# Performance work log

Measured on AMD Instinct MI355X. Metric: run time of the kernel, lower is better.

Reference implementation:

```python
import jax, jax.numpy as jnp
import numpy as np

N_NODES = 10000
N_EDGES = 320000
HIDDEN = 256
HEADS = 8
HEAD_DIM = HIDDEN // HEADS  # 32
NEG_SLOPE = 0.2


def setup_inputs() -> dict:
    key = jax.random.key(0)
    ks = jax.random.split(key, 12)
    x = jax.random.normal(ks[0], (N_NODES, HIDDEN), dtype=jnp.float32)
    edges_idx = jax.random.randint(ks[1], (2, N_EDGES), 0, N_NODES, dtype=jnp.int64)
    s = 1.0 / np.sqrt(HIDDEN)
    # layer 1 params
    W1 = jax.random.normal(ks[2], (HIDDEN, HEADS * HEAD_DIM), dtype=jnp.float32) * s
    a_src1 = jax.random.normal(ks[3], (HEADS, HEAD_DIM), dtype=jnp.float32) * s
    a_dst1 = jax.random.normal(ks[4], (HEADS, HEAD_DIM), dtype=jnp.float32) * s
    b1 = jnp.zeros((HEADS * HEAD_DIM,), dtype=jnp.float32)
    # layer 2 params
    W2 = jax.random.normal(ks[5], (HIDDEN, HEADS * HEAD_DIM), dtype=jnp.float32) * s
    a_src2 = jax.random.normal(ks[6], (HEADS, HEAD_DIM), dtype=jnp.float32) * s
    a_dst2 = jax.random.normal(ks[7], (HEADS, HEAD_DIM), dtype=jnp.float32) * s
    b2 = jnp.zeros((HEADS * HEAD_DIM,), dtype=jnp.float32)
    return {"x": x, "edges_idx": edges_idx,
            "W1": W1, "a_src1": a_src1, "a_dst1": a_dst1, "b1": b1,
            "W2": W2, "a_src2": a_src2, "a_dst2": a_dst2, "b2": b2}


def gat_conv(x, src, dst, W, a_src, a_dst, b):
    """PyG GATConv (concat=True, negative_slope=0.2), dropout in eval mode."""
    N = x.shape[0]
    h = (x @ W).reshape(N, HEADS, HEAD_DIM)          # [N,H,C]
    alpha_s = jnp.einsum('nhc,hc->nh', h, a_src)     # [N,H]
    alpha_d = jnp.einsum('nhc,hc->nh', h, a_dst)     # [N,H]
    e = alpha_s[src] + alpha_d[dst]                  # [E,H]
    e = jnp.where(e > 0, e, NEG_SLOPE * e)           # leaky_relu
    # scatter-softmax over incoming edges of each dst node
    m = jax.ops.segment_max(e, dst, num_segments=N)  # [N,H]
    ex = jnp.exp(e - m[dst])                         # [E,H]
    denom = jax.ops.segment_sum(ex, dst, num_segments=N)  # [N,H]
    alpha = ex / (denom[dst] + 1e-16)                # [E,H]
    msg = h[src] * alpha[:, :, None]                 # [E,H,C]
    out = jax.ops.segment_sum(msg, dst, num_segments=N)   # [N,H,C]
    return out.reshape(N, HEADS * HEAD_DIM) + b


def reference(x, edges_idx, W1, a_src1, a_dst1, b1, W2, a_src2, a_dst2, b2):
    src = edges_idx[0]
    dst = edges_idx[1]
    h = gat_conv(x, src, dst, W1, a_src1, a_dst1, b1)
    h = jax.nn.elu(h)
    out = gat_conv(h, src, dst, W2, a_src2, a_dst2, b2)
    return out
```

## Files before the change

kernel.cpp:

```cpp
#include <hip/hip_runtime.h>
#include <hip/hip_bf16.h>
#include <hip/hip_fp16.h>

#define N_NODES 10000
#define N_EDGES 320000
#define HIDDEN 256
#define HEADS 8
#define HEAD_DIM 32
#define NEG_SLOPE 0.2f
#define CAP 80

typedef __attribute__((ext_vector_type(8))) short short8;
typedef __attribute__((ext_vector_type(8))) _Float16 half8;
typedef __attribute__((ext_vector_type(4))) float f32x4;

__device__ __forceinline__ void bf16_split(float v, unsigned short& hi, unsigned short& lo) {
    __hip_bfloat16 hb = __float2bfloat16(v);
    float hf = __bfloat162float(hb);
    __hip_bfloat16 lb = __float2bfloat16(v - hf);
    hi = *reinterpret_cast<unsigned short*>(&hb);
    lo = *reinterpret_cast<unsigned short*>(&lb);
}

__global__ __launch_bounds__(256) void prep_kernel(
    const float* __restrict__ W1, const float* __restrict__ W2,
    const int* __restrict__ src, const int* __restrict__ dst,
    unsigned short* __restrict__ w1h, unsigned short* __restrict__ w1l,
    unsigned short* __restrict__ w2h, unsigned short* __restrict__ w2l,
    int* __restrict__ counts, int* __restrict__ csr_src) {
    int b = blockIdx.x;
    int tid = threadIdx.x;
    if (b < 512) {
        int i = b * 256 + tid;
        int which = i >> 16;
        int rem = i & 0xFFFF;
        int k = rem >> 8, n = rem & 255;
        const float* W = which ? W2 : W1;
        unsigned short* wh = which ? w2h : w1h;
        unsigned short* wl = which ? w2l : w1l;
        unsigned short h, l;
        bf16_split(W[k * 256 + n], h, l);
        wh[n * 256 + k] = h;
        wl[n * 256 + k] = l;
    } else {
        int e = (b - 512) * 256 + tid;
        int d = dst[e];
        int rank = atomicAdd(&counts[d], 1);
        csr_src[d * CAP + rank] = src[e];
    }
}

template <int AFP32>
__global__ __launch_bounds__(512) void gemm_mfma_kernel(
    const float* __restrict__ Axf,
    const unsigned short* __restrict__ Ah, const unsigned short* __restrict__ Al,
    const unsigned short* __restrict__ BhT, const unsigned short* __restrict__ BlT,
    _Float16* __restrict__ hH, const float* __restrict__ a_src,
    const float* __restrict__ a_dst, float* __restrict__ alpha_s,
    float* __restrict__ alpha_d) {
    __shared__ __align__(16) char smem[147968];
    unsigned short* sAh = (unsigned short*)smem;
    unsigned short* sAl = (unsigned short*)(smem + 6400);
    unsigned short* sBh = (unsigned short*)(smem + 12800);
    unsigned short* sBl = (unsigned short*)(smem + 80384);
    _Float16* sOut = (_Float16*)(smem + 12800);

    const int tid = threadIdx.x;
    const int w = tid >> 6, lane = tid & 63;
    const int c = w & 3, g = w >> 2;
    const int rtbase = g ? 3 : 0, nrt = g ? 2 : 3;
    const int col = lane & 15, quad = lane >> 4;
    const int m0 = blockIdx.y * 80, n0 = blockIdx.x * 128;

    f32x4 acc[3][2] = {};
    float4 raf[2][2];
    uint4 rau[2][2];

#define LOAD_A(k0, SS)                                                          \
    if (AFP32) {                                                                \
        _Pragma("unroll") for (int i = 0; i < 2; ++i) {                         \
            int t = tid + i * 512;                                              \
            if (t < 640) {                                                      \
                int row = t >> 3, seg = t & 7;                                  \
                raf[SS][i] = *(const float4*)&Axf[(size_t)(m0 + row) * 256 + (k0) + seg * 4]; \
            }                                                                   \
        }                                                                       \
    } else {                                                                    \
        _Pragma("unroll") for (int i = 0; i < 2; ++i) {                         \
            int t = tid + i * 512;                                              \
            if (t < 640) {                                                      \
                int tt = t < 320 ? t : t - 320;                                 \
                int row = tt >> 2, seg = tt & 3;                                \
                const unsigned short* P = t < 320 ? Ah : Al;                    \
                rau[SS][i] = *(const uint4*)&P[(size_t)(m0 + row) * 256 + (k0) + seg * 8]; \
            }                                                                   \
        }                                                                       \
    }
#define WRITE_A(SS)                                                             \
    if (AFP32) {                                                                \
        _Pragma("unroll") for (int i = 0; i < 2; ++i) {                         \
            int t = tid + i * 512;                                              \
            if (t < 640) {                                                      \
                int row = t >> 3, seg = t & 7;                                  \
                float4 v = raf[SS][i];                                          \
                ushort4 hh, ll;                                                 \
                unsigned short hb, lb;                                          \
                bf16_split(v.x, hb, lb); hh.x = hb; ll.x = lb;                  \
                bf16_split(v.y, hb, lb); hh.y = hb; ll.y = lb;                  \
                bf16_split(v.z, hb, lb); hh.z = hb; ll.z = lb;                  \
                bf16_split(v.w, hb, lb); hh.w = hb; ll.w = lb;                  \
                *(ushort4*)&sAh[row * 40 + seg * 4] = hh;                       \
                *(ushort4*)&sAl[row * 40 + seg * 4] = ll;                       \
            }                                                                   \
        }                                                                       \
    } else {                                                                    \
        _Pragma("unroll") for (int i = 0; i < 2; ++i) {                         \
            int t = tid + i * 512;                                              \
            if (t < 640) {                                                      \
                int tt = t < 320 ? t : t - 320;                                 \
                int row = tt >> 2, seg = tt & 3;                                \
                unsigned short* Sp = t < 320 ? sAh : sAl;                       \
                *(uint4*)&Sp[row * 40 + seg * 8] = rau[SS][i];                  \
            }                                                                   \
        }                                                                       \
    }

    LOAD_A(0, 0)
    LOAD_A(32, 1)

    {
        uint4 rbh[8], rbl[8];
#pragma unroll
        for (int i = 0; i < 8; ++i) {
            int chunk = tid + i * 512;
            int row = chunk >> 5, ks8 = chunk & 31;
            rbh[i] = *(const uint4*)&BhT[(size_t)(n0 + row) * 256 + ks8 * 8];
            rbl[i] = *(const uint4*)&BlT[(size_t)(n0 + row) * 256 + ks8 * 8];
        }
#pragma unroll
        for (int i = 0; i < 8; ++i) {
            int chunk = tid + i * 512;
            int row = chunk >> 5, ks8 = chunk & 31;
            *(uint4*)&sBh[row * 264 + ks8 * 8] = rbh[i];
            *(uint4*)&sBl[row * 264 + ks8 * 8] = rbl[i];
        }
    }

#pragma unroll
    for (int ks = 0; ks < 8; ++ks) {
        WRITE_A(ks & 1)
        __syncthreads();

        if (ks < 6) {
            LOAD_A((ks + 2) * 32, ks & 1)
        }

        const int kb = ks * 32 + quad * 8;
        short8 bh0 = *(const short8*)&sBh[(c * 32 + col) * 264 + kb];
        short8 bl0 = *(const short8*)&sBl[(c * 32 + col) * 264 + kb];
        short8 bh1 = *(const short8*)&sBh[(c * 32 + 16 + col) * 264 + kb];
        short8 bl1 = *(const short8*)&sBl[(c * 32 + 16 + col) * 264 + kb];
#pragma unroll
        for (int rt = 0; rt < 3; ++rt) {
            if (rt < nrt) {
                int rg = rtbase + rt;
                short8 ah = *(const short8*)&sAh[(rg * 16 + col) * 40 + quad * 8];
                short8 al = *(const short8*)&sAl[(rg * 16 + col) * 40 + quad * 8];
                acc[rt][0] = __builtin_amdgcn_mfma_f32_16x16x32_bf16(ah, bh0, acc[rt][0], 0, 0, 0);
                acc[rt][0] = __builtin_amdgcn_mfma_f32_16x16x32_bf16(ah, bl0, acc[rt][0], 0, 0, 0);
                acc[rt][0] = __builtin_amdgcn_mfma_f32_16x16x32_bf16(al, bh0, acc[rt][0], 0, 0, 0);
                acc[rt][1] = __builtin_amdgcn_mfma_f32_16x16x32_bf16(ah, bh1, acc[rt][1], 0, 0, 0);
                acc[rt][1] = __builtin_amdgcn_mfma_f32_16x16x32_bf16(ah, bl1, acc[rt][1], 0, 0, 0);
                acc[rt][1] = __builtin_amdgcn_mfma_f32_16x16x32_bf16(al, bh1, acc[rt][1], 0, 0, 0);
            }
        }
        __syncthreads();
    }
#undef LOAD_A
#undef WRITE_A

    const int head = blockIdx.x * 4 + c;
    float as0 = a_src[n0 + c * 32 + col];
    float as1 = a_src[n0 + c * 32 + 16 + col];
    float ad0 = a_dst[n0 + c * 32 + col];
    float ad1 = a_dst[n0 + c * 32 + 16 + col];
#pragma unroll
    for (int rt = 0; rt < 3; ++rt) {
        if (rt < nrt) {
            int rg = rtbase + rt;
#pragma unroll
            for (int r = 0; r < 4; ++r) {
                int row = rg * 16 + quad * 4 + r;
                sOut[row * 264 + c * 32 + col]      = (_Float16)acc[rt][0][r];
                sOut[row * 264 + c * 32 + 16 + col] = (_Float16)acc[rt][1][r];
                float ps = acc[rt][0][r] * as0 + acc[rt][1][r] * as1;
                float pd = acc[rt][0][r] * ad0 + acc[rt][1][r] * ad1;
#pragma unroll
                for (int m = 1; m < 16; m <<= 1) {
                    ps += __shfl_xor(ps, m);
                    pd += __shfl_xor(pd, m);
                }
                if (col == 0) {
                    int gm = m0 + row;
                    alpha_s[gm * HEADS + head] = ps;
                    alpha_d[gm * HEADS + head] = pd;
                }
            }
        }
    }
    __syncthreads();
#pragma unroll
    for (int i = 0; i < 3; ++i) {
        int t = tid + i * 512;
        if (t < 1280) {
            int row = t >> 4, seg = t & 15;
            *(half8*)&hH[(size_t)(m0 + row) * 256 + n0 + seg * 8] =
                *(const half8*)&sOut[row * 264 + seg * 8];
        }
    }
}

__global__ __launch_bounds__(256) void aggregate_kernel(
    const int* __restrict__ counts, const int* __restrict__ csr_src,
    const float* __restrict__ alpha_s, const float* __restrict__ alpha_d,
    const _Float16* __restrict__ hH, const float* __restrict__ bias,
    float* __restrict__ outf, unsigned short* __restrict__ oh,
    unsigned short* __restrict__ ol, int mode) {
    const int tid = threadIdx.x;
    const int w = tid >> 6, lane = tid & 63;
    const int d = blockIdx.x * 4 + w;
    const int q = lane >> 4, fl = lane & 15;
    const int hd0 = fl >> 2, hd1 = 4 + (fl >> 2);
    const int qb = q * 4;
    const int* __restrict__ bucket = csr_src + d * CAP;
    const _Float16* hp0 = hH + fl * 8;
    const _Float16* hp1 = hH + 128 + fl * 8;

    const int n = counts[d];
    const float ad0 = alpha_d[d * HEADS + hd0];
    const float ad1 = alpha_d[d * HEADS + hd1];
    int4 s0_ = *(const int4*)&bucket[qb];
    int4 s1_ = *(const int4*)&bucket[qb + 16];
    int4 s2_ = *(const int4*)&bucket[qb + 32];
    int4 s3_ = *(const int4*)&bucket[qb + 48];

    float accA[8] = {}, accB[8] = {};
    float denA = 0.f, denB = 0.f;

#define AGG_DECL(t) float aA##t##0, aA##t##1, aA##t##2, aA##t##3;               \
                    float aB##t##0, aB##t##1, aB##t##2, aB##t##3;               \
                    half8 hA##t##0, hA##t##1, hA##t##2, hA##t##3;               \
                    half8 hB##t##0, hB##t##1, hB##t##2, hB##t##3;
    AGG_DECL(0) AGG_DECL(1) AGG_DECL(2) AGG_DECL(3) AGG_DECL(4)

#define AGG_CLAMP(x) ((x) < 0 ? 0 : ((x) > 9999 ? 9999 : (x)))
#define AGG_GATHER(t, sv)                                                       \
    {                                                                           \
        int i0_ = AGG_CLAMP((sv).x), i1_ = AGG_CLAMP((sv).y);                   \
        int i2_ = AGG_CLAMP((sv).z), i3_ = AGG_CLAMP((sv).w);                   \
        aA##t##0 = alpha_s[i0_ * HEADS + hd0];                                  \
        aA##t##1 = alpha_s[i1_ * HEADS + hd0];                                  \
        aA##t##2 = alpha_s[i2_ * HEADS + hd0];                                  \
        aA##t##3 = alpha_s[i3_ * HEADS + hd0];                                  \
        aB##t##0 = alpha_s[i0_ * HEADS + hd1];                                  \
        aB##t##1 = alpha_s[i1_ * HEADS + hd1];                                  \
        aB##t##2 = alpha_s[i2_ * HEADS + hd1];                                  \
        aB##t##3 = alpha_s[i3_ * HEADS + hd1];                                  \
        hA##t##0 = *(const half8*)&hp0[(size_t)i0_ * HIDDEN];                   \
        hA##t##1 = *(const half8*)&hp0[(size_t)i1_ * HIDDEN];                   \
        hA##t##2 = *(const half8*)&hp0[(size_t)i2_ * HIDDEN];                   \
        hA##t##3 = *(const half8*)&hp0[(size_t)i3_ * HIDDEN];                   \
        hB##t##0 = *(const half8*)&hp1[(size_t)i0_ * HIDDEN];                   \
        hB##t##1 = *(const half8*)&hp1[(size_t)i1_ * HIDDEN];                   \
        hB##t##2 = *(const half8*)&hp1[(size_t)i2_ * HIDDEN];                   \
        hB##t##3 = *(const half8*)&hp1[(size_t)i3_ * HIDDEN];                   \
    }
#define AGG_COMPUTE(t, base)                                                    \
    {                                                                           \
        int b0_ = (base) + qb;                                                  \
        float eA0 = aA##t##0 + ad0; eA0 = eA0 > 0.f ? eA0 : NEG_SLOPE * eA0;    \
        float eA1 = aA##t##1 + ad0; eA1 = eA1 > 0.f ? eA1 : NEG_SLOPE * eA1;    \
        float eA2 = aA##t##2 + ad0; eA2 = eA2 > 0.f ? eA2 : NEG_SLOPE * eA2;    \
        float eA3 = aA##t##3 + ad0; eA3 = eA3 > 0.f ? eA3 : NEG_SLOPE * eA3;    \
        float eB0 = aB##t##0 + ad1; eB0 = eB0 > 0.f ? eB0 : NEG_SLOPE * eB0;    \
        float eB1 = aB##t##1 + ad1; eB1 = eB1 > 0.f ? eB1 : NEG_SLOPE * eB1;    \
        float eB2 = aB##t##2 + ad1; eB2 = eB2 > 0.f ? eB2 : NEG_SLOPE * eB2;    \
        float eB3 = aB##t##3 + ad1; eB3 = eB3 > 0.f ? eB3 : NEG_SLOPE * eB3;    \
        if (b0_ >= n)     { eA0 = -1e30f; eB0 = -1e30f; }                       \
        if (b0_ + 1 >= n) { eA1 = -1e30f; eB1 = -1e30f; }                       \
        if (b0_ + 2 >= n) { eA2 = -1e30f; eB2 = -1e30f; }                       \
        if (b0_ + 3 >= n) { eA3 = -1e30f; eB3 = -1e30f; }                       \
        float vA0 = __expf(eA0), vA1 = __expf(eA1);                             \
        float vA2 = __expf(eA2), vA3 = __expf(eA3);                             \
        float vB0 = __expf(eB0), vB1 = __expf(eB1);                             \
        float vB2 = __expf(eB2), vB3 = __expf(eB3);                             \
        denA += (vA0 + vA1) + (vA2 + vA3);                                      \
        denB += (vB0 + vB1) + (vB2 + vB3);                                      \
        _Pragma("unroll") for (int j = 0; j < 8; ++j)                           \
            accA[j] += (float)hA##t##0[j] * vA0 + (float)hA##t##1[j] * vA1 +    \
                       (float)hA##t##2[j] * vA2 + (float)hA##t##3[j] * vA3;     \
        _Pragma("unroll") for (int j = 0; j < 8; ++j)                           \
            accB[j] += (float)hB##t##0[j] * vB0 + (float)hB##t##1[j] * vB1 +    \
                       (float)hB##t##2[j] * vB2 + (float)hB##t##3[j] * vB3;     \
    }

    if (n > 0)  AGG_GATHER(0, s0_)
    if (n > 16) AGG_GATHER(1, s1_)
    if (n > 0)  AGG_COMPUTE(0, 0)
    if (n > 32) AGG_GATHER(2, s2_)
    if (n > 16) AGG_COMPUTE(1, 16)
    if (n > 48) AGG_GATHER(3, s3_)
    if (n > 32) AGG_COMPUTE(2, 32)
    if (n > 48) AGG_COMPUTE(3, 48)
    if (n > 64) {
        int4 s4_ = *(const int4*)&bucket[qb + 64];
        AGG_GATHER(4, s4_)
        AGG_COMPUTE(4, 64)
    }

#undef AGG_DECL
#undef AGG_CLAMP
#undef AGG_GATHER
#undef AGG_COMPUTE

#pragma unroll
    for (int j = 0; j < 8; ++j) {
        accA[j] += __shfl_xor(accA[j], 16);
        accB[j] += __shfl_xor(accB[j], 16);
    }
    denA += __shfl_xor(denA, 16);
    denB += __shfl_xor(denB, 16);
#pragma unroll
    for (int j = 0; j < 8; ++j) {
        accA[j] += __shfl_xor(accA[j], 32);
        accB[j] += __shfl_xor(accB[j], 32);
    }
    denA += __shfl_xor(denA, 32);
    denB += __shfl_xor(denB, 32);

    if (q == 0) {
        float invA = 1.f / (denA + 1e-16f);
        float invB = 1.f / (denB + 1e-16f);
        float vA[8], vB[8];
#pragma unroll
        for (int j = 0; j < 8; ++j) {
            vA[j] = accA[j] * invA + bias[fl * 8 + j];
            vB[j] = accB[j] * invB + bias[128 + fl * 8 + j];
        }
        size_t o0 = (size_t)d * HIDDEN + fl * 8;
        size_t o1 = o0 + 128;
        if (mode == 1) {
            unsigned short hb[8], lb[8];
#pragma unroll
            for (int j = 0; j < 8; ++j) {
                vA[j] = vA[j] > 0.f ? vA[j] : (__expf(vA[j]) - 1.f);
                bf16_split(vA[j], hb[j], lb[j]);
            }
            *(ushort4*)&oh[o0]     = make_ushort4(hb[0], hb[1], hb[2], hb[3]);
            *(ushort4*)&oh[o0 + 4] = make_ushort4(hb[4], hb[5], hb[6], hb[7]);
            *(ushort4*)&ol[o0]     = make_ushort4(lb[0], lb[1], lb[2], lb[3]);
            *(ushort4*)&ol[o0 + 4] = make_ushort4(lb[4], lb[5], lb[6], lb[7]);
#pragma unroll
            for (int j = 0; j < 8; ++j) {
                vB[j] = vB[j] > 0.f ? vB[j] : (__expf(vB[j]) - 1.f);
                bf16_split(vB[j], hb[j], lb[j]);
            }
            *(ushort4*)&oh[o1]     = make_ushort4(hb[0], hb[1], hb[2], hb[3]);
            *(ushort4*)&oh[o1 + 4] = make_ushort4(hb[4], hb[5], hb[6], hb[7]);
            *(ushort4*)&ol[o1]     = make_ushort4(lb[0], lb[1], lb[2], lb[3]);
            *(ushort4*)&ol[o1 + 4] = make_ushort4(lb[4], lb[5], lb[6], lb[7]);
        } else {
            *(float4*)&outf[o0]     = make_float4(vA[0], vA[1], vA[2], vA[3]);
            *(float4*)&outf[o0 + 4] = make_float4(vA[4], vA[5], vA[6], vA[7]);
            *(float4*)&outf[o1]     = make_float4(vB[0], vB[1], vB[2], vB[3]);
            *(float4*)&outf[o1 + 4] = make_float4(vB[4], vB[5], vB[6], vB[7]);
        }
    }
}

extern "C" void kernel_launch(void* const* d_in, const int* in_sizes, int n_in,
                              void* d_out, int out_size, void* d_ws, size_t ws_size,
                              hipStream_t stream) {
    const float* x      = (const float*)d_in[0];
    const int*   edges  = (const int*)d_in[1];
    const float* W1     = (const float*)d_in[2];
    const float* as1    = (const float*)d_in[3];
    const float* ad1    = (const float*)d_in[4];
    const float* b1     = (const float*)d_in[5];
    const float* W2     = (const float*)d_in[6];
    const float* as2    = (const float*)d_in[7];
    const float* ad2    = (const float*)d_in[8];
    const float* b2     = (const float*)d_in[9];
    float* out = (float*)d_out;

    const int* src = edges;
    const int* dst = edges + N_EDGES;

    const size_t NF = (size_t)N_NODES * HIDDEN;
    const size_t NH = (size_t)N_NODES * HEADS;

    char* base = (char*)d_ws;
    _Float16* hH = (_Float16*)base;             base += NF * 2;
    unsigned short* x2h = (unsigned short*)base; base += NF * 2;
    unsigned short* x2l = (unsigned short*)base; base += NF * 2;
    float* alpha_s = (float*)base;              base += NH * 4;
    float* alpha_d = (float*)base;              base += NH * 4;
    unsigned short* w1h = (unsigned short*)base; base += 65536 * 2;
    unsigned short* w1l = (unsigned short*)base; base += 65536 * 2;
    unsigned short* w2h = (unsigned short*)base; base += 65536 * 2;
    unsigned short* w2l = (unsigned short*)base; base += 65536 * 2;
    int* csr_src = (int*)base;                  base += (size_t)N_NODES * CAP * 4;
    int* counts  = (int*)base;                  base += (size_t)N_NODES * 4;

    dim3 gemm_grid(2, 125);
    const int EB = (N_EDGES + 255) / 256;
    const int AGG_B = 2500;

    hipMemsetAsync(counts, 0, N_NODES * sizeof(int), stream);
    prep_kernel<<<512 + EB, 256, 0, stream>>>(W1, W2, src, dst,
                                              w1h, w1l, w2h, w2l, counts, csr_src);

    gemm_mfma_kernel<1><<<gemm_grid, 512, 0, stream>>>(
        x, nullptr, nullptr, w1h, w1l, hH, as1, ad1, alpha_s, alpha_d);
    aggregate_kernel<<<AGG_B, 256, 0, stream>>>(counts, csr_src, alpha_s, alpha_d,
                                                hH, b1, nullptr, x2h, x2l, 1);

    gemm_mfma_kernel<0><<<gemm_grid, 512, 0, stream>>>(
        nullptr, x2h, x2l, w2h, w2l, hH, as2, ad2, alpha_s, alpha_d);
    aggregate_kernel<<<AGG_B, 256, 0, stream>>>(counts, csr_src, alpha_s, alpha_d,
                                                hH, b2, out, nullptr, nullptr, 0);
}
```

Measured before the change: 181.0 us.

## Double-buffer A tile in LDS with 4-deep register prefetch in GEMM

Restructures the GEMM k-loop so the A tile is double-buffered in shared memory and global loads are prefetched four stages ahead in registers. Each step writes the next A slice while computing the current one, leaving one barrier per step instead of two. This aims to hide global-load and LDS-write latency behind MFMA work. In exchange it uses more LDS (about 157 KB) and more registers, which could lower occupancy or cause spills.

```diff
diff --git a/kernel.cpp b/kernel.cpp
--- a/kernel.cpp
+++ b/kernel.cpp
@@ -58,12 +58,14 @@
     _Float16* __restrict__ hH, const float* __restrict__ a_src,
     const float* __restrict__ a_dst, float* __restrict__ alpha_s,
     float* __restrict__ alpha_d) {
-    __shared__ __align__(16) char smem[147968];
-    unsigned short* sAh = (unsigned short*)smem;
-    unsigned short* sAl = (unsigned short*)(smem + 6400);
-    unsigned short* sBh = (unsigned short*)(smem + 12800);
-    unsigned short* sBl = (unsigned short*)(smem + 80384);
-    _Float16* sOut = (_Float16*)(smem + 12800);
+    __shared__ __align__(16) char smem[160768];
+    unsigned short* sAh0 = (unsigned short*)smem;
+    unsigned short* sAl0 = (unsigned short*)(smem + 6400);
+    unsigned short* sAh1 = (unsigned short*)(smem + 12800);
+    unsigned short* sAl1 = (unsigned short*)(smem + 19200);
+    unsigned short* sBh  = (unsigned short*)(smem + 25600);
+    unsigned short* sBl  = (unsigned short*)(smem + 93184);
+    _Float16* sOut = (_Float16*)(smem + 25600);
 
     const int tid = threadIdx.x;
     const int w = tid >> 6, lane = tid & 63;
@@ -73,8 +75,8 @@
     const int m0 = blockIdx.y * 80, n0 = blockIdx.x * 128;
 
     f32x4 acc[3][2] = {};
-    float4 raf[2][2];
-    uint4 rau[2][2];
+    float4 raf[4][2];
+    uint4 rau[4][2];
 
 #define LOAD_A(k0, SS)                                                          \
     if (AFP32) {                                                                \
@@ -96,37 +98,69 @@
             }                                                                   \
         }                                                                       \
     }
-#define WRITE_A(SS)                                                             \
-    if (AFP32) {                                                                \
-        _Pragma("unroll") for (int i = 0; i < 2; ++i) {                         \
-            int t = tid + i * 512;                                              \
-            if (t < 640) {                                                      \
-                int row = t >> 3, seg = t & 7;                                  \
-                float4 v = raf[SS][i];                                          \
-                ushort4 hh, ll;                                                 \
-                unsigned short hb, lb;                                          \
-                bf16_split(v.x, hb, lb); hh.x = hb; ll.x = lb;                  \
-                bf16_split(v.y, hb, lb); hh.y = hb; ll.y = lb;                  \
-                bf16_split(v.z, hb, lb); hh.z = hb; ll.z = lb;                  \
-                bf16_split(v.w, hb, lb); hh.w = hb; ll.w = lb;                  \
-                *(ushort4*)&sAh[row * 40 + seg * 4] = hh;                       \
-                *(ushort4*)&sAl[row * 40 + seg * 4] = ll;                       \
+#define WRITE_A(SS, BUF)                                                        \
+    {                                                                           \
+        unsigned short* dh_ = (BUF) ? sAh1 : sAh0;                              \
+        unsigned short* dl_ = (BUF) ? sAl1 : sAl0;                              \
+        if (AFP32) {                                                            \
+            _Pragma("unroll") for (int i = 0; i < 2; ++i) {                     \
+                int t = tid + i * 512;                                          \
+                if (t < 640) {                                                  \
+                    int row = t >> 3, seg = t & 7;                              \
+                    float4 v = raf[SS][i];                                      \
+                    ushort4 hh, ll;                                             \
+                    unsigned short hb, lb;                                      \
+                    bf16_split(v.x, hb, lb); hh.x = hb; ll.x = lb;              \
+                    bf16_split(v.y, hb, lb); hh.y = hb; ll.y = lb;              \
+                    bf16_split(v.z, hb, lb); hh.z = hb; ll.z = lb;              \
+                    bf16_split(v.w, hb, lb); hh.w = hb; ll.w = lb;              \
+                    *(ushort4*)&dh_[row * 40 + seg * 4] = hh;                   \
+                    *(ushort4*)&dl_[row * 40 + seg * 4] = ll;                   \
+                }                                                               \
+            }                                                                   \
+        } else {                                                                \
+            _Pragma("unroll") for (int i = 0; i < 2; ++i) {                     \
+                int t = tid + i * 512;                                          \
+                if (t < 640) {                                                  \
+                    int tt = t < 320 ? t : t - 320;                             \
+                    int row = tt >> 2, seg = tt & 3;                            \
+                    unsigned short* Sp = t < 320 ? dh_ : dl_;                   \
+                    *(uint4*)&Sp[row * 40 + seg * 8] = rau[SS][i];              \
+                }                                                               \
             }                                                                   \
         }                                                                       \
-    } else {                                                                    \
-        _Pragma("unroll") for (int i = 0; i < 2; ++i) {                         \
-            int t = tid + i * 512;                                              \
-            if (t < 640) {                                                      \
-                int tt = t < 320 ? t : t - 320;                                 \
-                int row = tt >> 2, seg = tt & 3;                                \
-                unsigned short* Sp = t < 320 ? sAh : sAl;                       \
-                *(uint4*)&Sp[row * 40 + seg * 8] = rau[SS][i];                  \
+    }
+#define COMPUTE(ks)                                                             \
+    {                                                                           \
+        const unsigned short* ah_ = ((ks) & 1) ? sAh1 : sAh0;                   \
+        const unsigned short* al_ = ((ks) & 1) ? sAl1 : sAl0;                   \
+        const int kb = (ks) * 32 + quad * 8;                                    \
+        short8 bh0 = *(const short8*)&sBh[(c * 32 + col) * 264 + kb];           \
+        short8 bl0 = *(const short8*)&sBl[(c * 32 + col) * 264 + kb];           \
+        short8 bh1 = *(const short8*)&sBh[(c * 32 + 16 + col) * 264 + kb];      \
+        short8 bl1 = *(const short8*)&sBl[(c * 32 + 16 + col) * 264 + kb];      \
+        _Pragma("unroll") for (int rt = 0; rt < 3; ++rt) {                      \
+            if (rt < nrt) {                                                     \
+                int rg = rtbase + rt;                                           \
+                short8 ah = *(const short8*)&ah_[(rg * 16 + col) * 40 + quad * 8]; \
+                short8 al = *(const short8*)&al_[(rg * 16 + col) * 40 + quad * 8]; \
+                acc[rt][0] = __builtin_amdgcn_mfma_f32_16x16x32_bf16(ah, bh0, acc[rt][0], 0, 0, 0); \
+                acc[rt][0] = __builtin_amdgcn_mfma_f32_16x16x32_bf16(ah, bl0, acc[rt][0], 0, 0, 0); \
+                acc[rt][0] = __builtin_amdgcn_mfma_f32_16x16x32_bf16(al, bh0, acc[rt][0], 0, 0, 0); \
+                acc[rt][1] = __builtin_amdgcn_mfma_f32_16x16x32_bf16(ah, bh1, acc[rt][1], 0, 0, 0); \
+                acc[rt][1] = __builtin_amdgcn_mfma_f32_16x16x32_bf16(ah, bl1, acc[rt][1], 0, 0, 0); \
+                acc[rt][1] = __builtin_amdgcn_mfma_f32_16x16x32_bf16(al, bh1, acc[rt][1], 0, 0, 0); \
             }                                                                   \
         }                                                                       \
     }
 
     LOAD_A(0, 0)
     LOAD_A(32, 1)
+    LOAD_A(64, 2)
+    LOAD_A(96, 3)
+
+    WRITE_A(0, 0)
+    LOAD_A(128, 0)
 
     {
         uint4 rbh[8], rbl[8];
@@ -145,39 +179,27 @@
             *(uint4*)&sBl[row * 264 + ks8 * 8] = rbl[i];
         }
     }
-
-#pragma unroll
-    for (int ks = 0; ks < 8; ++ks) {
-        WRITE_A(ks & 1)
-        __syncthreads();
-
-        if (ks < 6) {
-            LOAD_A((ks + 2) * 32, ks & 1)
-        }
-
-        const int kb = ks * 32 + quad * 8;
-        short8 bh0 = *(const short8*)&sBh[(c * 32 + col) * 264 + kb];
-        short8 bl0 = *(const short8*)&sBl[(c * 32 + col) * 264 + kb];
-        short8 bh1 = *(const short8*)&sBh[(c * 32 + 16 + col) * 264 + kb];
-        short8 bl1 = *(const short8*)&sBl[(c * 32 + 16 + col) * 264 + kb];
-#pragma unroll
-        for (int rt = 0; rt < 3; ++rt) {
-            if (rt < nrt) {
-                int rg = rtbase + rt;
-                short8 ah = *(const short8*)&sAh[(rg * 16 + col) * 40 + quad * 8];
-                short8 al = *(const short8*)&sAl[(rg * 16 + col) * 40 + quad * 8];
-                acc[rt][0] = __builtin_amdgcn_mfma_f32_16x16x32_bf16(ah, bh0, acc[rt][0], 0, 0, 0);
-                acc[rt][0] = __builtin_amdgcn_mfma_f32_16x16x32_bf16(ah, bl0, acc[rt][0], 0, 0, 0);
-                acc[rt][0] = __builtin_amdgcn_mfma_f32_16x16x32_bf16(al, bh0, acc[rt][0], 0, 0, 0);
-                acc[rt][1] = __builtin_amdgcn_mfma_f32_16x16x32_bf16(ah, bh1, acc[rt][1], 0, 0, 0);
-                acc[rt][1] = __builtin_amdgcn_mfma_f32_16x16x32_bf16(ah, bl1, acc[rt][1], 0, 0, 0);
-                acc[rt][1] = __builtin_amdgcn_mfma_f32_16x16x32_bf16(al, bh1, acc[rt][1], 0, 0, 0);
-            }
-        }
-        __syncthreads();
-    }
+    __syncthreads();
+
+#define STEP(ks, REFILL)                                                        \
+    WRITE_A((ks + 1) & 3, (ks + 1) & 1)                                         \
+    if (REFILL) { LOAD_A((ks + 5) * 32, (ks + 1) & 3) }                         \
+    COMPUTE(ks)                                                                 \
+    __syncthreads();
+
+    STEP(0, 1)
+    STEP(1, 1)
+    STEP(2, 1)
+    STEP(3, 0)
+    STEP(4, 0)
+    STEP(5, 0)
+    STEP(6, 0)
+    COMPUTE(7)
+    __syncthreads();
+#undef STEP
 #undef LOAD_A
 #undef WRITE_A
+#undef COMPUTE
 
     const int head = blockIdx.x * 4 + c;
     float as0 = a_src[n0 + c * 32 + col];
```

Result: no change. 180.1 us (-0.5%).

## Halve GEMM block N-tile to 64 with 256 threads; tile weight transpose via LDS

Applied to the files above, without the earlier changes.

The GEMM now uses 64-column tiles and 256-thread blocks, giving a 4x125 grid. This halves shared memory per block (about 80KB instead of 148KB), so more blocks can be resident and the 125-row GEMM fills more CUs. The A tile is now loaded separately by each of twice as many blocks, which adds redundant global traffic. Separately, the weight bf16 split/transpose prep uses 64x64 LDS tiles with coalesced float4 reads and vector writes instead of scattered per-element transposed stores.

```diff
diff --git a/kernel.cpp b/kernel.cpp
--- a/kernel.cpp
+++ b/kernel.cpp
@@ -30,20 +30,40 @@
     int* __restrict__ counts, int* __restrict__ csr_src) {
     int b = blockIdx.x;
     int tid = threadIdx.x;
-    if (b < 512) {
-        int i = b * 256 + tid;
-        int which = i >> 16;
-        int rem = i & 0xFFFF;
-        int k = rem >> 8, n = rem & 255;
+    if (b < 32) {
+        __shared__ unsigned short sh[64][66], sl[64][66];
+        const int which = b >> 4, tile = b & 15;
+        const int kt = (tile >> 2) * 64, nt = (tile & 3) * 64;
         const float* W = which ? W2 : W1;
         unsigned short* wh = which ? w2h : w1h;
         unsigned short* wl = which ? w2l : w1l;
-        unsigned short h, l;
-        bf16_split(W[k * 256 + n], h, l);
-        wh[n * 256 + k] = h;
-        wl[n * 256 + k] = l;
+        {
+            const int kl = tid >> 2, ns = (tid & 3) * 16;
+#pragma unroll
+            for (int j = 0; j < 16; j += 4) {
+                float4 v = *(const float4*)&W[(size_t)(kt + kl) * 256 + nt + ns + j];
+                unsigned short h_, l_;
+                bf16_split(v.x, h_, l_); sh[kl][ns + j]     = h_; sl[kl][ns + j]     = l_;
+                bf16_split(v.y, h_, l_); sh[kl][ns + j + 1] = h_; sl[kl][ns + j + 1] = l_;
+                bf16_split(v.z, h_, l_); sh[kl][ns + j + 2] = h_; sl[kl][ns + j + 2] = l_;
+                bf16_split(v.w, h_, l_); sh[kl][ns + j + 3] = h_; sl[kl][ns + j + 3] = l_;
+            }
+        }
+        __syncthreads();
+        {
+            const int nl = tid >> 2, ks = (tid & 3) * 16;
+            unsigned short oh_[16], ol_[16];
+#pragma unroll
+            for (int j = 0; j < 16; ++j) { oh_[j] = sh[ks + j][nl]; ol_[j] = sl[ks + j][nl]; }
+            size_t base = (size_t)(nt + nl) * 256 + kt + ks;
+#pragma unroll
+            for (int j = 0; j < 16; j += 4) {
+                *(ushort4*)&wh[base + j] = make_ushort4(oh_[j], oh_[j+1], oh_[j+2], oh_[j+3]);
+                *(ushort4*)&wl[base + j] = make_ushort4(ol_[j], ol_[j+1], ol_[j+2], ol_[j+3]);
+            }
+        }
     } else {
-        int e = (b - 512) * 256 + tid;
+        int e = (b - 32) * 256 + tid;
         int d = dst[e];
         int rank = atomicAdd(&counts[d], 1);
         csr_src[d * CAP + rank] = src[e];
@@ -51,43 +71,43 @@
 }
 
 template <int AFP32>
-__global__ __launch_bounds__(512) void gemm_mfma_kernel(
+__global__ __launch_bounds__(256) void gemm_mfma_kernel(
     const float* __restrict__ Axf,
     const unsigned short* __restrict__ Ah, const unsigned short* __restrict__ Al,
     const unsigned short* __restrict__ BhT, const unsigned short* __restrict__ BlT,
     _Float16* __restrict__ hH, const float* __restrict__ a_src,
     const float* __restrict__ a_dst, float* __restrict__ alpha_s,
     float* __restrict__ alpha_d) {
-    __shared__ __align__(16) char smem[147968];
+    __shared__ __align__(16) char smem[80384];
     unsigned short* sAh = (unsigned short*)smem;
     unsigned short* sAl = (unsigned short*)(smem + 6400);
     unsigned short* sBh = (unsigned short*)(smem + 12800);
-    unsigned short* sBl = (unsigned short*)(smem + 80384);
+    unsigned short* sBl = (unsigned short*)(smem + 46592);
     _Float16* sOut = (_Float16*)(smem + 12800);
 
     const int tid = threadIdx.x;
     const int w = tid >> 6, lane = tid & 63;
-    const int c = w & 3, g = w >> 2;
+    const int c = w & 1, g = w >> 1;
     const int rtbase = g ? 3 : 0, nrt = g ? 2 : 3;
     const int col = lane & 15, quad = lane >> 4;
-    const int m0 = blockIdx.y * 80, n0 = blockIdx.x * 128;
+    const int m0 = blockIdx.y * 80, n0 = blockIdx.x * 64;
 
     f32x4 acc[3][2] = {};
-    float4 raf[2][2];
-    uint4 rau[2][2];
+    float4 raf[2][3];
+    uint4 rau[2][3];
 
 #define LOAD_A(k0, SS)                                                          \
     if (AFP32) {                                                                \
-        _Pragma("unroll") for (int i = 0; i < 2; ++i) {                         \
-            int t = tid + i * 512;                                              \
+        _Pragma("unroll") for (int i = 0; i < 3; ++i) {                         \
+            int t = tid + i * 256;                                              \
             if (t < 640) {                                                      \
                 int row = t >> 3, seg = t & 7;                                  \
                 raf[SS][i] = *(const float4*)&Axf[(size_t)(m0 + row) * 256 + (k0) + seg * 4]; \
             }                                                                   \
         }                                                                       \
     } else {                                                                    \
-        _Pragma("unroll") for (int i = 0; i < 2; ++i) {                         \
-            int t = tid + i * 512;                                              \
+        _Pragma("unroll") for (int i = 0; i < 3; ++i) {                         \
+            int t = tid + i * 256;                                              \
             if (t < 640) {                                                      \
                 int tt = t < 320 ? t : t - 320;                                 \
                 int row = tt >> 2, seg = tt & 3;                                \
@@ -98,8 +118,8 @@
     }
 #define WRITE_A(SS)                                                             \
     if (AFP32) {                                                                \
-        _Pragma("unroll") for (int i = 0; i < 2; ++i) {                         \
-            int t = tid + i * 512;                                              \
+        _Pragma("unroll") for (int i = 0; i < 3; ++i) {                         \
+            int t = tid + i * 256;                                              \
             if (t < 640) {                                                      \
                 int row = t >> 3, seg = t & 7;                                  \
                 float4 v = raf[SS][i];                                          \
@@ -114,8 +134,8 @@
             }                                                                   \
         }                                                                       \
     } else {                                                                    \
-        _Pragma("unroll") for (int i = 0; i < 2; ++i) {                         \
-            int t = tid + i * 512;                                              \
+        _Pragma("unroll") for (int i = 0; i < 3; ++i) {                         \
+            int t = tid + i * 256;                                              \
             if (t < 640) {                                                      \
                 int tt = t < 320 ? t : t - 320;                                 \
                 int row = tt >> 2, seg = tt & 3;                                \
@@ -124,6 +144,27 @@
             }                                                                   \
         }                                                                       \
     }
+#define COMPUTE(ks)                                                             \
+    {                                                                           \
+        const int kb = (ks) * 32 + quad * 8;                                    \
+        short8 bh0 = *(const short8*)&sBh[(c * 32 + col) * 264 + kb];           \
+        short8 bl0 = *(const short8*)&sBl[(c * 32 + col) * 264 + kb];           \
+        short8 bh1 = *(const short8*)&sBh[(c * 32 + 16 + col) * 264 + kb];      \
+        short8 bl1 = *(const short8*)&sBl[(c * 32 + 16 + col) * 264 + kb];      \
+        _Pragma("unroll") for (int rt = 0; rt < 3; ++rt) {                      \
+            if (rt < nrt) {                                                     \
+                int rg = rtbase + rt;                                           \
+                short8 ah = *(const short8*)&sAh[(rg * 16 + col) * 40 + quad * 8]; \
+                short8 al = *(const short8*)&sAl[(rg * 16 + col) * 40 + quad * 8]; \
+                acc[rt][0] = __builtin_amdgcn_mfma_f32_16x16x32_bf16(ah, bh0, acc[rt][0], 0, 0, 0); \
+                acc[rt][0] = __builtin_amdgcn_mfma_f32_16x16x32_bf16(ah, bl0, acc[rt][0], 0, 0, 0); \
+                acc[rt][0] = __builtin_amdgcn_mfma_f32_16x16x32_bf16(al, bh0, acc[rt][0], 0, 0, 0); \
+                acc[rt][1] = __builtin_amdgcn_mfma_f32_16x16x32_bf16(ah, bh1, acc[rt][1], 0, 0, 0); \
+                acc[rt][1] = __builtin_amdgcn_mfma_f32_16x16x32_bf16(ah, bl1, acc[rt][1], 0, 0, 0); \
+                acc[rt][1] = __builtin_amdgcn_mfma_f32_16x16x32_bf16(al, bh1, acc[rt][1], 0, 0, 0); \
+            }                                                                   \
+        }                                                                       \
+    }
 
     LOAD_A(0, 0)
     LOAD_A(32, 1)
@@ -132,14 +173,14 @@
         uint4 rbh[8], rbl[8];
 #pragma unroll
         for (int i = 0; i < 8; ++i) {
-            int chunk = tid + i * 512;
+            int chunk = tid + i * 256;
             int row = chunk >> 5, ks8 = chunk & 31;
             rbh[i] = *(const uint4*)&BhT[(size_t)(n0 + row) * 256 + ks8 * 8];
             rbl[i] = *(const uint4*)&BlT[(size_t)(n0 + row) * 256 + ks8 * 8];
         }
 #pragma unroll
         for (int i = 0; i < 8; ++i) {
-            int chunk = tid + i * 512;
+            int chunk = tid + i * 256;
             int row = chunk >> 5, ks8 = chunk & 31;
             *(uint4*)&sBh[row * 264 + ks8 * 8] = rbh[i];
             *(uint4*)&sBl[row * 264 + ks8 * 8] = rbl[i];
@@ -155,31 +196,14 @@
             LOAD_A((ks + 2) * 32, ks & 1)
         }
 
-        const int kb = ks * 32 + quad * 8;
-        short8 bh0 = *(const short8*)&sBh[(c * 32 + col) * 264 + kb];
-        short8 bl0 = *(const short8*)&sBl[(c * 32 + col) * 264 + kb];
-        short8 bh1 = *(const short8*)&sBh[(c * 32 + 16 + col) * 264 + kb];
-        short8 bl1 = *(const short8*)&sBl[(c * 32 + 16 + col) * 264 + kb];
-#pragma unroll
-        for (int rt = 0; rt < 3; ++rt) {
-            if (rt < nrt) {
-                int rg = rtbase + rt;
-                short8 ah = *(const short8*)&sAh[(rg * 16 + col) * 40 + quad * 8];
-                short8 al = *(const short8*)&sAl[(rg * 16 + col) * 40 + quad * 8];
-                acc[rt][0] = __builtin_amdgcn_mfma_f32_16x16x32_bf16(ah, bh0, acc[rt][0], 0, 0, 0);
-                acc[rt][0] = __builtin_amdgcn_mfma_f32_16x16x32_bf16(ah, bl0, acc[rt][0], 0, 0, 0);
-                acc[rt][0] = __builtin_amdgcn_mfma_f32_16x16x32_bf16(al, bh0, acc[rt][0], 0, 0, 0);
-                acc[rt][1] = __builtin_amdgcn_mfma_f32_16x16x32_bf16(ah, bh1, acc[rt][1], 0, 0, 0);
-                acc[rt][1] = __builtin_amdgcn_mfma_f32_16x16x32_bf16(ah, bl1, acc[rt][1], 0, 0, 0);
-                acc[rt][1] = __builtin_amdgcn_mfma_f32_16x16x32_bf16(al, bh1, acc[rt][1], 0, 0, 0);
-            }
-        }
+        COMPUTE(ks)
         __syncthreads();
     }
 #undef LOAD_A
 #undef WRITE_A
-
-    const int head = blockIdx.x * 4 + c;
+#undef COMPUTE
+
+    const int head = blockIdx.x * 2 + c;
     float as0 = a_src[n0 + c * 32 + col];
     float as1 = a_src[n0 + c * 32 + 16 + col];
     float ad0 = a_dst[n0 + c * 32 + col];
@@ -191,8 +215,8 @@
 #pragma unroll
             for (int r = 0; r < 4; ++r) {
                 int row = rg * 16 + quad * 4 + r;
-                sOut[row * 264 + c * 32 + col]      = (_Float16)acc[rt][0][r];
-                sOut[row * 264 + c * 32 + 16 + col] = (_Float16)acc[rt][1][r];
+                sOut[row * 72 + c * 32 + col]      = (_Float16)acc[rt][0][r];
+                sOut[row * 72 + c * 32 + 16 + col] = (_Float16)acc[rt][1][r];
                 float ps = acc[rt][0][r] * as0 + acc[rt][1][r] * as1;
                 float pd = acc[rt][0][r] * ad0 + acc[rt][1][r] * ad1;
 #pragma unroll
@@ -211,11 +235,11 @@
     __syncthreads();
 #pragma unroll
     for (int i = 0; i < 3; ++i) {
-        int t = tid + i * 512;
-        if (t < 1280) {
-            int row = t >> 4, seg = t & 15;
+        int t = tid + i * 256;
+        if (t < 640) {
+            int row = t >> 3, seg = t & 7;
             *(half8*)&hH[(size_t)(m0 + row) * 256 + n0 + seg * 8] =
-                *(const half8*)&sOut[row * 264 + seg * 8];
+                *(const half8*)&sOut[row * 72 + seg * 8];
         }
     }
 }
@@ -412,20 +436,20 @@
     int* csr_src = (int*)base;                  base += (size_t)N_NODES * CAP * 4;
     int* counts  = (int*)base;                  base += (size_t)N_NODES * 4;
 
-    dim3 gemm_grid(2, 125);
+    dim3 gemm_grid(4, 125);
     const int EB = (N_EDGES + 255) / 256;
     const int AGG_B = 2500;
 
     hipMemsetAsync(counts, 0, N_NODES * sizeof(int), stream);
-    prep_kernel<<<512 + EB, 256, 0, stream>>>(W1, W2, src, dst,
-                                              w1h, w1l, w2h, w2l, counts, csr_src);
-
-    gemm_mfma_kernel<1><<<gemm_grid, 512, 0, stream>>>(
+    prep_kernel<<<32 + EB, 256, 0, stream>>>(W1, W2, src, dst,
+                                             w1h, w1l, w2h, w2l, counts, csr_src);
+
+    gemm_mfma_kernel<1><<<gemm_grid, 256, 0, stream>>>(
         x, nullptr, nullptr, w1h, w1l, hH, as1, ad1, alpha_s, alpha_d);
     aggregate_kernel<<<AGG_B, 256, 0, stream>>>(counts, csr_src, alpha_s, alpha_d,
                                                 hH, b1, nullptr, x2h, x2l, 1);
 
-    gemm_mfma_kernel<0><<<gemm_grid, 512, 0, stream>>>(
+    gemm_mfma_kernel<0><<<gemm_grid, 256, 0, stream>>>(
         nullptr, x2h, x2l, w2h, w2l, hH, as2, ad2, alpha_s, alpha_d);
     aggregate_kernel<<<AGG_B, 256, 0, stream>>>(counts, csr_src, alpha_s, alpha_d,
                                                 hH, b2, out, nullptr, nullptr, 0);
```

After: 187.3 us. 1.03x slower.
